# Kernel optimization log

Measured on AMD Instinct MI355X. Metric: run time of the kernel, lower is better.

## Reference

```python
import jax, jax.numpy as jnp
import numpy as np

VOCAB, D, A, NEG = 32000, 200, 20, 2
NUM_USERS, NUM_ITEMS = 100000, 50000
R, L, B, NNZ = 4096, 128, 1024, 20480
EPS = 1e-12

def _norm(x, axis):
    n = jnp.sqrt(jnp.sum(x * x, axis=axis, keepdims=True))
    return x / jnp.maximum(n, EPS)

def setup_inputs() -> dict:
    key = jax.random.key(0)
    ks = jax.random.split(key, 20)
    rows_u = jax.random.randint(ks[5], (NNZ,), 0, B)
    cols_u = jax.random.randint(ks[6], (NNZ,), 0, R)
    rows_i = jax.random.randint(ks[7], (NNZ,), 0, B)
    cols_i = jax.random.randint(ks[8], (NNZ,), 0, R)
    return {
        "historical_review": jax.random.randint(ks[0], (R, L), 0, VOCAB),
        "neg_review": jax.random.randint(ks[1], (R * NEG, L), 0, VOCAB),
        "user": jax.random.randint(ks[2], (B,), 0, NUM_USERS),
        "item": jax.random.randint(ks[3], (B,), 0, NUM_ITEMS),
        "label": jax.random.uniform(ks[4], (B,), jnp.float32, 1.0, 5.0),
        "user_histor_index": jnp.stack([rows_u, cols_u]),
        "user_histor_value": jax.random.uniform(ks[9], (NNZ,), jnp.float32),
        "item_histor_index": jnp.stack([rows_i, cols_i]),
        "item_histor_value": jax.random.uniform(ks[10], (NNZ,), jnp.float32),
        "word_emb": jax.random.normal(ks[11], (VOCAB, D), jnp.float32),
        "Wm": jax.random.normal(ks[12], (D, D), jnp.float32) * 0.05,
        "Ww": jax.random.normal(ks[13], (A, D), jnp.float32) * 0.05,
        "bw": jnp.zeros((A,), jnp.float32),
        "Wt": jax.random.normal(ks[14], (D, A), jnp.float32) * 0.05,
        "fc_w": jax.random.uniform(ks[15], (1, 2 * D), jnp.float32, -0.05, 0.05),
        "fc_b": jnp.zeros((1,), jnp.float32),
        "fm_V": jax.random.uniform(ks[16], (2 * D, 10), jnp.float32, -0.05, 0.05),
        "b_users": jax.random.uniform(ks[17], (NUM_USERS, 1), jnp.float32, 0.0, 0.1),
        "b_items": jax.random.uniform(ks[18], (NUM_ITEMS, 1), jnp.float32, 0.0, 0.1),
    }

def reference(historical_review, neg_review, user, item, label,
              user_histor_index, user_histor_value,
              item_histor_index, item_histor_value,
              word_emb, Wm, Ww, bw, Wt, fc_w, fc_b, fm_V, b_users, b_items):
    # ABAE attention over each review
    e_w = word_emb[historical_review]              # (R, L, D)
    y_s = jnp.mean(e_w, axis=1)                    # (R, D)
    z_n = jnp.mean(word_emb[neg_review], axis=1)   # (R*NEG, D)
    dx = jnp.einsum('rld,rd->rl', e_w @ Wm.T, y_s) # (R, L)
    ax = jax.nn.softmax(dx, axis=1)
    # Faithful to source: view(R, D, L) is a raw reshape, not a transpose.
    z_s = jnp.einsum('rdl,rl->rd', e_w.reshape(R, D, L), ax)  # (R, D)
    p_t = z_s @ Ww.T + bw                          # (R, A)
    r_s = p_t @ Wt.T                               # (R, D)
    # cosine margin ranking loss
    c1 = jnp.sum(_norm(r_s, 1) * _norm(z_s, 1), axis=-1)      # (R,)
    c1 = jnp.repeat(c1, NEG)                                   # (R*NEG,)
    c2 = jnp.sum(_norm(z_n.reshape(R, NEG, D), 2) * _norm(r_s, 1)[:, None, :], axis=-1).reshape(-1)
    abae_out_loss = jax.nn.relu(c2 - c1 + 1.0)     # margin=1, target=+1
    J_loss = jnp.mean(abae_out_loss)
    # aspect-matrix orthogonality regularizer
    Tn = _norm(Wt, 0)                              # normalize columns (dim=0)
    U_loss = jnp.mean((Tn.T @ Tn - jnp.eye(A, dtype=Wt.dtype)) ** 2)
    # sparse (B, R) @ (R, D) aggregation via segment_sum
    user_aspect_embed = jax.ops.segment_sum(
        user_histor_value[:, None] * r_s[user_histor_index[1]],
        user_histor_index[0], num_segments=B)      # (B, D)
    item_aspect_embed = jax.ops.segment_sum(
        item_histor_value[:, None] * r_s[item_histor_index[1]],
        item_histor_index[0], num_segments=B)      # (B, D)
    input_vec = jnp.concatenate([user_aspect_embed, item_aspect_embed], axis=1)  # (B, 2D)
    fm_linear = input_vec @ fc_w.T + fc_b          # (B, 1)
    fm_i1 = (input_vec @ fm_V) ** 2
    fm_i2 = (input_vec ** 2) @ (fm_V ** 2)
    # NOTE: faithful to source, the quadratic term is summed over the whole batch (scalar)
    fm_output = 0.5 * jnp.sum(fm_i1 - fm_i2) + fm_linear + b_users[user] + b_items[item]
    prediction = fm_output.squeeze(1)              # (B,)
    rating_loss = (prediction - label) ** 2
    mse_loss = jnp.mean(rating_loss)
    obj_loss = mse_loss + 0.01 * J_loss + 0.01 * U_loss
    return (obj_loss, rating_loss, abae_out_loss, prediction, user_aspect_embed, item_aspect_embed)
```

## Files before the change

### kernel.cpp

```cpp
#include <hip/hip_runtime.h>
#include <hip/hip_fp16.h>
#include <math.h>

#define R_TOT 4096
#define L_LEN 128
#define D_DIM 200
#define A_DIM 20
#define NEGK  2
#define B_SZ  1024
#define NNZ_C 20480
#define RN_TOT (R_TOT*NEGK)
#define S_TOT (R_TOT + RN_TOT)
#define VOCAB_C 32000
#define VHALF 16000
#define EPS_ 1e-12f
#define SLOT_CAP 64
#define NBUCK_BLK 160

__device__ __forceinline__ float4 unpack4(const uint2 u) {
  union { unsigned v; __half2 h; } c0, c1;
  c0.v = u.x; c1.v = u.y;
  const float2 f0 = __half22float2(c0.h);
  const float2 f1 = __half22float2(c1.h);
  return make_float4(f0.x, f0.y, f1.x, f1.y);
}

typedef _Float16 h2v __attribute__((ext_vector_type(2)));
__device__ __forceinline__ float fdot2u(unsigned a, unsigned b, float c) {
  union { unsigned u; h2v h; } ua, ub;
  ua.u = a; ub.u = b;
  return __builtin_amdgcn_fdot2(ua.h, ub.h, c, false);
}
__device__ __forceinline__ float dot8f(const uint4 q, const uint4 w, float c) {
  float s = c;
  s = fdot2u(q.x, w.x, s); s = fdot2u(q.y, w.y, s);
  s = fdot2u(q.z, w.z, s); s = fdot2u(q.w, w.w, s);
  return s;
}

#define DPPI(old_, src_, ctrl, rmask) \
  __builtin_amdgcn_update_dpp(old_, src_, ctrl, rmask, 0xf, false)

__device__ __forceinline__ float dpp_sum32(float s) {
  s += __int_as_float(DPPI(0, __float_as_int(s), 0x111, 0xf));
  s += __int_as_float(DPPI(0, __float_as_int(s), 0x112, 0xf));
  s += __int_as_float(DPPI(0, __float_as_int(s), 0x114, 0xf));
  s += __int_as_float(DPPI(0, __float_as_int(s), 0x118, 0xf));
  s += __int_as_float(DPPI(0, __float_as_int(s), 0x142, 0xa));
  return s;
}
__device__ __forceinline__ float dpp_sum64(float s) {
  s = dpp_sum32(s);
  s += __int_as_float(DPPI(0, __float_as_int(s), 0x143, 0xc));
  return s;
}
__device__ __forceinline__ float dpp_max64(float s) {
  s = fmaxf(s, __int_as_float(DPPI(__float_as_int(s), __float_as_int(s), 0x111, 0xf)));
  s = fmaxf(s, __int_as_float(DPPI(__float_as_int(s), __float_as_int(s), 0x112, 0xf)));
  s = fmaxf(s, __int_as_float(DPPI(__float_as_int(s), __float_as_int(s), 0x114, 0xf)));
  s = fmaxf(s, __int_as_float(DPPI(__float_as_int(s), __float_as_int(s), 0x118, 0xf)));
  s = fmaxf(s, __int_as_float(DPPI(__float_as_int(s), __float_as_int(s), 0x142, 0xa)));
  s = fmaxf(s, __int_as_float(DPPI(__float_as_int(s), __float_as_int(s), 0x143, 0xc)));
  return s;
}

__global__ __launch_bounds__(256) void k_cast(
    const float* __restrict__ emb, ushort* __restrict__ emb_h, int* __restrict__ cnt)
{
  if (blockIdx.x == 0) {
    for (int i = threadIdx.x; i < 2*B_SZ; i += 256) cnt[i] = 0;
  }
  const int idx = blockIdx.x*256 + threadIdx.x;
  if (idx < (VOCAB_C*D_DIM)/4) {
    const float4 v = reinterpret_cast<const float4*>(emb)[idx];
    ushort4 o;
    o.x = __half_as_ushort(__float2half(v.x));
    o.y = __half_as_ushort(__float2half(v.y));
    o.z = __half_as_ushort(__float2half(v.z));
    o.w = __half_as_ushort(__float2half(v.w));
    reinterpret_cast<ushort4*>(emb_h)[idx] = o;
  }
}

#define ACC8M(Q, M) { \
  const float4 e0_ = unpack4(make_uint2((Q).x,(Q).y)); \
  const float4 e1_ = unpack4(make_uint2((Q).z,(Q).w)); \
  sA.x = fmaf(M, e0_.x, sA.x); sA.y = fmaf(M, e0_.y, sA.y); \
  sA.z = fmaf(M, e0_.z, sA.z); sA.w = fmaf(M, e0_.w, sA.w); \
  sB.x = fmaf(M, e1_.x, sB.x); sB.y = fmaf(M, e1_.y, sB.y); \
  sB.z = fmaf(M, e1_.z, sB.z); sB.w = fmaf(M, e1_.w, sB.w); }

__global__ __launch_bounds__(256, 8) void k_means_phase(
    const int* __restrict__ hist, const int* __restrict__ neg,
    const ushort* __restrict__ emb_h,
    float* __restrict__ ys_all, float* __restrict__ zn_all,
    const int* __restrict__ uidx, const float* __restrict__ uval,
    const int* __restrict__ iidx, const float* __restrict__ ival,
    int* __restrict__ cnt, int* __restrict__ scol, float* __restrict__ sval,
    int lo, int finalize)
{
  const int sb = blockIdx.x;
  const int tid = threadIdx.x;

  if (sb >= S_TOT) {
    const int g = (sb - S_TOT)*256 + tid;
    if (g < NNZ_C) {
      const int b = uidx[g];
      const int slot = atomicAdd(&cnt[b], 1);
      if (slot < SLOT_CAP) {
        scol[b*SLOT_CAP + slot] = uidx[NNZ_C + g];
        sval[b*SLOT_CAP + slot] = uval[g];
      }
    } else {
      const int g2 = g - NNZ_C;
      const int b = iidx[g2];
      const int slot = atomicAdd(&cnt[B_SZ + b], 1);
      if (slot < SLOT_CAP) {
        scol[(B_SZ + b)*SLOT_CAP + slot] = iidx[NNZ_C + g2];
        sval[(B_SZ + b)*SLOT_CAP + slot] = ival[g2];
      }
    }
    return;
  }

  __shared__ int widx[L_LEN];
  __shared__ __align__(16) float part[8][D_DIM];
  const bool is_pos = (sb < R_TOT);
  const int* src = is_pos ? (hist + (size_t)sb*L_LEN)
                          : (neg + (size_t)(sb - R_TOT)*L_LEN);
  if (tid < L_LEN) widx[tid] = src[tid];
  __syncthreads();

  const int c5 = tid & 31;
  const int j  = tid >> 5;
  float4 sA = {0.f,0.f,0.f,0.f}, sB = {0.f,0.f,0.f,0.f};
  if (c5 < 25) {
    const size_t coff = 8*c5;
    #pragma unroll
    for (int half = 0; half < 2; ++half) {
      const int base = j + 64*half;
      int   wv_[8]; float m_[8];
      #pragma unroll
      for (int k = 0; k < 8; ++k) {
        const int w = widx[base + 8*k];
        const bool in = ((unsigned)(w - lo) < (unsigned)VHALF);
        wv_[k] = in ? w : 0;
        m_[k]  = in ? 1.f : 0.f;
      }
      const uint4 q0 = *reinterpret_cast<const uint4*>(emb_h + (size_t)wv_[0]*D_DIM + coff);
      const uint4 q1 = *reinterpret_cast<const uint4*>(emb_h + (size_t)wv_[1]*D_DIM + coff);
      const uint4 q2 = *reinterpret_cast<const uint4*>(emb_h + (size_t)wv_[2]*D_DIM + coff);
      const uint4 q3 = *reinterpret_cast<const uint4*>(emb_h + (size_t)wv_[3]*D_DIM + coff);
      const uint4 q4 = *reinterpret_cast<const uint4*>(emb_h + (size_t)wv_[4]*D_DIM + coff);
      const uint4 q5 = *reinterpret_cast<const uint4*>(emb_h + (size_t)wv_[5]*D_DIM + coff);
      const uint4 q6 = *reinterpret_cast<const uint4*>(emb_h + (size_t)wv_[6]*D_DIM + coff);
      const uint4 q7 = *reinterpret_cast<const uint4*>(emb_h + (size_t)wv_[7]*D_DIM + coff);
      ACC8M(q0, m_[0]) ACC8M(q1, m_[1]) ACC8M(q2, m_[2]) ACC8M(q3, m_[3])
      ACC8M(q4, m_[4]) ACC8M(q5, m_[5]) ACC8M(q6, m_[6]) ACC8M(q7, m_[7])
    }
    *reinterpret_cast<float4*>(&part[j][8*c5])     = sA;
    *reinterpret_cast<float4*>(&part[j][8*c5 + 4]) = sB;
  }
  __syncthreads();
  float* dst = is_pos ? (ys_all + (size_t)sb*D_DIM)
                      : (zn_all + (size_t)(sb - R_TOT)*D_DIM);
  if (tid < D_DIM) {
    float a = 0.f;
    #pragma unroll
    for (int j2 = 0; j2 < 8; ++j2) a += part[j2][tid];
    if (finalize) dst[tid] = (dst[tid] + a) * (1.0f/128.0f);
    else          dst[tid] = a;
  }
}

#define KB_RT 16
__global__ __launch_bounds__(256, 2) void k_matvec(
    const float* __restrict__ ys_all, const float* __restrict__ Wm,
    ushort* __restrict__ vvh)
{
  __shared__ float ysl[KB_RT][D_DIM];
  const int r0 = blockIdx.x * KB_RT;
  const int tid = threadIdx.x;
  for (int i = tid; i < KB_RT*D_DIM; i += 256)
    ysl[i / D_DIM][i % D_DIM] = ys_all[(size_t)r0*D_DIM + i];
  __syncthreads();
  if (tid < D_DIM) {
    float acc[KB_RT];
    #pragma unroll
    for (int r = 0; r < KB_RT; ++r) acc[r] = 0.f;
    #pragma unroll 4
    for (int k = 0; k < D_DIM; ++k) {
      const float w = Wm[k*D_DIM + tid];
      #pragma unroll
      for (int r = 0; r < KB_RT; ++r) acc[r] += ysl[r][k] * w;
    }
    #pragma unroll
    for (int r = 0; r < KB_RT; ++r)
      vvh[(size_t)(r0 + r)*D_DIM + tid] = __half_as_ushort(__float2half(acc[r]));
  }
}

__global__ __launch_bounds__(512, 8) void k_attn(
    const int* __restrict__ hist, const ushort* __restrict__ emb_h,
    const ushort* __restrict__ vvh,
    const float* __restrict__ Ww, const float* __restrict__ bw,
    const float* __restrict__ Wt, const float* __restrict__ zn_all,
    float* __restrict__ rs_out, float* __restrict__ abae)
{
  __shared__ __align__(16) float part[D_DIM][17];
  __shared__ __align__(16) float ax[L_LEN];
  __shared__ __align__(16) ushort axh[L_LEN];
  __shared__ __align__(16) float zs[D_DIM];
  __shared__ __align__(16) float ubuf[240];
  int*   widx  = reinterpret_cast<int*>(ubuf);
  float* ptile = ubuf;
  float* red   = ubuf + 160;

  const int r = blockIdx.x;
  const int tid = threadIdx.x, lane = tid & 63, wv = tid >> 6;
  const int c5 = tid & 31;
  const int j  = tid >> 5;
  const bool act = (c5 < 25);
  const int coff = 8*c5;

  if (tid < L_LEN) widx[tid] = hist[r*L_LEN + tid];
  uint4 v8u = make_uint4(0,0,0,0);
  if (act) v8u = *reinterpret_cast<const uint4*>(vvh + (size_t)r*D_DIM + coff);
  __syncthreads();

  uint4 q0,q1,q2,q3,q4,q5,q6,q7;
  q0=q1=q2=q3=q4=q5=q6=q7=make_uint4(0,0,0,0);
  float zn0 = 0.f, zn1 = 0.f;
  float p0=0.f,p1=0.f,p2=0.f,p3=0.f,p4=0.f,p5=0.f,p6=0.f,p7=0.f;
  if (act) {
    q0 = *reinterpret_cast<const uint4*>(emb_h + (size_t)widx[j +   0]*D_DIM + coff);
    q1 = *reinterpret_cast<const uint4*>(emb_h + (size_t)widx[j +  16]*D_DIM + coff);
    q2 = *reinterpret_cast<const uint4*>(emb_h + (size_t)widx[j +  32]*D_DIM + coff);
    q3 = *reinterpret_cast<const uint4*>(emb_h + (size_t)widx[j +  48]*D_DIM + coff);
    q4 = *reinterpret_cast<const uint4*>(emb_h + (size_t)widx[j +  64]*D_DIM + coff);
    q5 = *reinterpret_cast<const uint4*>(emb_h + (size_t)widx[j +  80]*D_DIM + coff);
    q6 = *reinterpret_cast<const uint4*>(emb_h + (size_t)widx[j +  96]*D_DIM + coff);
    q7 = *reinterpret_cast<const uint4*>(emb_h + (size_t)widx[j + 112]*D_DIM + coff);
  }
  if (tid < D_DIM) {
    zn0 = zn_all[(size_t)(2*r)*D_DIM + tid];
    zn1 = zn_all[(size_t)(2*r + 1)*D_DIM + tid];
  }
  if (act) {
    p0 = dot8f(q0, v8u, 0.f); p1 = dot8f(q1, v8u, 0.f);
    p2 = dot8f(q2, v8u, 0.f); p3 = dot8f(q3, v8u, 0.f);
    p4 = dot8f(q4, v8u, 0.f); p5 = dot8f(q5, v8u, 0.f);
    p6 = dot8f(q6, v8u, 0.f); p7 = dot8f(q7, v8u, 0.f);
  }
  p0 = dpp_sum32(p0); p1 = dpp_sum32(p1); p2 = dpp_sum32(p2); p3 = dpp_sum32(p3);
  p4 = dpp_sum32(p4); p5 = dpp_sum32(p5); p6 = dpp_sum32(p6); p7 = dpp_sum32(p7);
  if (c5 == 31) {
    ax[j]      = p0; ax[j + 16]  = p1; ax[j + 32]  = p2; ax[j + 48]  = p3;
    ax[j + 64] = p4; ax[j + 80]  = p5; ax[j + 96]  = p6; ax[j + 112] = p7;
  }
  __syncthreads();

  float mx = fmaxf(ax[lane], ax[lane + 64]);
  mx = dpp_max64(mx);
  const float M = __int_as_float(__builtin_amdgcn_readlane(__float_as_int(mx), 63));

  if (tid < L_LEN) {
    const float e = expf(ax[tid] - M);
    axh[tid] = __half_as_ushort(__float2half(e));
    const float s = dpp_sum64(e);
    if (lane == 63) red[1 + wv] = s;
  }
  __syncthreads();

  if (act) {
    const int Y  = 25*j + c5;
    const int l0 = (8*Y) & 127;
    const int v0 = Y >> 4;
    const int sl = Y & 15;
    const uint4 ax8u = *reinterpret_cast<const uint4*>(axh + l0);
    part[v0 +   0][sl] = dot8f(q0, ax8u, 0.f);
    part[v0 +  25][sl] = dot8f(q1, ax8u, 0.f);
    part[v0 +  50][sl] = dot8f(q2, ax8u, 0.f);
    part[v0 +  75][sl] = dot8f(q3, ax8u, 0.f);
    part[v0 + 100][sl] = dot8f(q4, ax8u, 0.f);
    part[v0 + 125][sl] = dot8f(q5, ax8u, 0.f);
    part[v0 + 150][sl] = dot8f(q6, ax8u, 0.f);
    part[v0 + 175][sl] = dot8f(q7, ax8u, 0.f);
  }
  __syncthreads();

  if (tid < D_DIM) {
    const float Sinv = 1.0f / (red[1] + red[2]);
    float s = 0.f;
    #pragma unroll
    for (int i = 0; i < 16; ++i) s += part[tid][i];
    zs[tid] = s * Sinv;
  }
  __syncthreads();

  if (tid < 160) {
    const int a = tid % 20, jj = tid / 20;
    float s = 0.f;
    #pragma unroll
    for (int ii = 0; ii < 25; ++ii) {
      const int d = jj + 8*ii;
      s += zs[d] * Ww[a*D_DIM + d];
    }
    ptile[tid] = s;
  }
  __syncthreads();
  if (tid < A_DIM) {
    float s = bw[tid];
    #pragma unroll
    for (int jj = 0; jj < 8; ++jj) s += ptile[jj*20 + tid];
    red[2 + tid] = s;
  }
  __syncthreads();

  float rsd = 0.f, zsd = 0.f;
  if (tid < D_DIM) {
    float acc = 0.f;
    #pragma unroll
    for (int a = 0; a < A_DIM; ++a) acc += red[2+a] * Wt[tid*A_DIM + a];
    rsd = acc; zsd = zs[tid];
    rs_out[(size_t)r*D_DIM + tid] = acc;
  } else { zn0 = 0.f; zn1 = 0.f; }
  float a0 = dpp_sum64(rsd*rsd), a1 = dpp_sum64(zsd*zsd), a2 = dpp_sum64(rsd*zsd);
  float b0 = dpp_sum64(zn0*zn0), b1 = dpp_sum64(zn0*rsd);
  float b2 = dpp_sum64(zn1*zn1), b3 = dpp_sum64(zn1*rsd);
  if (lane == 63) {
    red[22 + 0*8 + wv] = a0; red[22 + 1*8 + wv] = a1; red[22 + 2*8 + wv] = a2;
    red[22 + 3*8 + wv] = b0; red[22 + 4*8 + wv] = b1;
    red[22 + 5*8 + wv] = b2; red[22 + 6*8 + wv] = b3;
  }
  __syncthreads();

  if (tid < 64) {
    const int qi = tid >> 3, k = tid & 7;
    float v = (qi < 7) ? red[22 + 8*qi + k] : 0.f;
    v += __shfl_xor(v, 1); v += __shfl_xor(v, 2); v += __shfl_xor(v, 4);
    const float s0 = __shfl(v, 0),  s1 = __shfl(v, 8),  s2 = __shfl(v, 16);
    const float t0 = __shfl(v, 24), t1 = __shfl(v, 32);
    const float t2 = __shfl(v, 40), t3 = __shfl(v, 48);
    if (tid == 0) {
      const float nr = fmaxf(sqrtf(s0), EPS_);
      const float nz = fmaxf(sqrtf(s1), EPS_);
      const float c1 = s2 / (nr * nz);
      const float c2a = t1 / (fmaxf(sqrtf(t0), EPS_) * nr);
      const float c2b = t3 / (fmaxf(sqrtf(t2), EPS_) * nr);
      abae[2*r]     = fmaxf(c2a - c1 + 1.0f, 0.0f);
      abae[2*r + 1] = fmaxf(c2b - c1 + 1.0f, 0.0f);
    }
  }
}

__global__ __launch_bounds__(512) void k_aggfm(
    const int* __restrict__ cnt, const int* __restrict__ scol,
    const float* __restrict__ sval, const float* __restrict__ rs,
    const float* __restrict__ fcw, const float* __restrict__ V,
    const float* __restrict__ Wt, const float* __restrict__ abae,
    float* __restrict__ uae, float* __restrict__ iae,
    float* __restrict__ linb, float* __restrict__ quadb,
    float* __restrict__ uj)
{
  __shared__ __align__(16) float ivec[2*D_DIM];
  __shared__ float redw[8];
  __shared__ float qpart[10];
  __shared__ float cninvS[A_DIM];
  const int b = blockIdx.x;
  const int tid = threadIdx.x, lane = tid & 63, wv = tid >> 6;

  if (b == B_SZ) {
    if (tid < 400) {
      const int a = tid / 20, c = tid % 20;
      float dot = 0.f;
      #pragma unroll 4
      for (int d = 0; d < D_DIM; ++d) dot += Wt[d*A_DIM + a] * Wt[d*A_DIM + c];
      ivec[tid] = dot;
    }
    __syncthreads();
    if (tid < A_DIM) cninvS[tid] = 1.0f / fmaxf(sqrtf(ivec[tid*21]), EPS_);
    __syncthreads();
    float u = 0.f;
    if (tid < 400) {
      const int a = tid / 20, c = tid % 20;
      const float g = ivec[tid]*cninvS[a]*cninvS[c] - (a==c ? 1.0f : 0.0f);
      u = g*g;
    }
    #pragma unroll
    for (int o = 32; o > 0; o >>= 1) u += __shfl_xor(u, o);
    if (lane == 0) redw[wv] = u;
    __syncthreads();
    if (tid == 0) {
      float s = 0.f;
      #pragma unroll
      for (int i = 0; i < 8; ++i) s += redw[i];
      uj[0] = s;
    }
    return;
  }
  if (b == B_SZ + 1) {
    float s = 0.f;
    for (int i = tid; i < RN_TOT; i += 512) s += abae[i];
    #pragma unroll
    for (int o = 32; o > 0; o >>= 1) s += __shfl_xor(s, o);
    if (lane == 0) redw[wv] = s;
    __syncthreads();
    if (tid == 0) {
      float t = 0.f;
      #pragma unroll
      for (int i = 0; i < 8; ++i) t += redw[i];
      uj[1] = t;
    }
    return;
  }

  if (tid < D_DIM) {
    int n = cnt[b]; n = n < SLOT_CAP ? n : SLOT_CAP;
    const int* cols = scol + (size_t)b*SLOT_CAP;
    const float* vals = sval + (size_t)b*SLOT_CAP;
    float acc = 0.f;
    for (int j = 0; j < n; ++j) acc += vals[j] * rs[(size_t)cols[j]*D_DIM + tid];
    ivec[tid] = acc;
    uae[(size_t)b*D_DIM + tid] = acc;
  } else if (tid >= 256 && tid < 256 + D_DIM) {
    const int t = tid - 256;
    int n = cnt[B_SZ + b]; n = n < SLOT_CAP ? n : SLOT_CAP;
    const int* cols = scol + (size_t)(B_SZ + b)*SLOT_CAP;
    const float* vals = sval + (size_t)(B_SZ + b)*SLOT_CAP;
    float acc = 0.f;
    for (int j = 0; j < n; ++j) acc += vals[j] * rs[(size_t)cols[j]*D_DIM + t];
    ivec[D_DIM + t] = acc;
    iae[(size_t)b*D_DIM + t] = acc;
  }
  __syncthreads();

  float lv = 0.f;
  if (tid < 2*D_DIM) lv = ivec[tid] * fcw[tid];
  #pragma unroll
  for (int o = 32; o > 0; o >>= 1) lv += __shfl_xor(lv, o);
  if (lane == 0) redw[wv] = lv;

  {
    const int k = wv;
    float s1 = 0.f, s2 = 0.f;
    for (int f = lane; f < 2*D_DIM; f += 64) {
      const float x = ivec[f];
      const float vk = V[f*10 + k];
      s1 += x*vk; s2 += x*x*vk*vk;
    }
    #pragma unroll
    for (int o = 32; o > 0; o >>= 1) { s1 += __shfl_xor(s1,o); s2 += __shfl_xor(s2,o); }
    if (lane == 0) qpart[k] = s1*s1 - s2;
  }
  if (wv < 2) {
    const int k = 8 + wv;
    float s1 = 0.f, s2 = 0.f;
    for (int f = lane; f < 2*D_DIM; f += 64) {
      const float x = ivec[f];
      const float vk = V[f*10 + k];
      s1 += x*vk; s2 += x*x*vk*vk;
    }
    #pragma unroll
    for (int o = 32; o > 0; o >>= 1) { s1 += __shfl_xor(s1,o); s2 += __shfl_xor(s2,o); }
    if (lane == 0) qpart[k] = s1*s1 - s2;
  }
  __syncthreads();
  if (tid == 0) {
    float lin = 0.f;
    #pragma unroll
    for (int i = 0; i < 8; ++i) lin += redw[i];
    float q = 0.f;
    #pragma unroll
    for (int i = 0; i < 10; ++i) q += qpart[i];
    linb[b] = lin; quadb[b] = q;
  }
}

__global__ __launch_bounds__(1024) void k_final2(
    const float* __restrict__ quadb, const float* __restrict__ linb,
    const float* __restrict__ fcb, const int* __restrict__ user,
    const int* __restrict__ item, const float* __restrict__ busers,
    const float* __restrict__ bitems, const float* __restrict__ label,
    const float* __restrict__ uj,
    float* __restrict__ pred, float* __restrict__ rl, float* __restrict__ obj)
{
  __shared__ float sA[16], sC[16];
  __shared__ float quad_s;
  const int tid = threadIdx.x;
  const int lane = tid & 63;
  const int wv = tid >> 6;

  float q = quadb[tid];
  #pragma unroll
  for (int o = 32; o > 0; o >>= 1) q += __shfl_xor(q, o);
  if (lane == 0) sA[wv] = q;
  __syncthreads();
  if (wv == 0) {
    float s = (lane < 16) ? sA[lane] : 0.f;
    #pragma unroll
    for (int o = 32; o > 0; o >>= 1) s += __shfl_xor(s, o);
    if (lane == 0) quad_s = s;
  }
  __syncthreads();

  const float p = 0.5f*quad_s + linb[tid] + fcb[0]
                + busers[user[tid]] + bitems[item[tid]];
  pred[tid] = p;
  const float dd = p - label[tid];
  const float myrl = dd*dd;
  rl[tid] = myrl;

  float ms = myrl;
  #pragma unroll
  for (int o = 32; o > 0; o >>= 1) ms += __shfl_xor(ms, o);
  if (lane == 0) sC[wv] = ms;
  __syncthreads();
  if (tid == 0) {
    float Ms = 0.f;
    for (int i = 0; i < 16; ++i) Ms += sC[i];
    obj[0] = Ms/1024.0f + 0.01f*(uj[1]/8192.0f) + 0.01f*(uj[0]/400.0f);
  }
}

extern "C" void kernel_launch(void* const* d_in, const int* in_sizes, int n_in,
                              void* d_out, int out_size, void* d_ws, size_t ws_size,
                              hipStream_t stream) {
  const int*   hist   = (const int*)  d_in[0];
  const int*   neg    = (const int*)  d_in[1];
  const int*   user   = (const int*)  d_in[2];
  const int*   item   = (const int*)  d_in[3];
  const float* label  = (const float*)d_in[4];
  const int*   uidx   = (const int*)  d_in[5];
  const float* uval   = (const float*)d_in[6];
  const int*   iidx   = (const int*)  d_in[7];
  const float* ival   = (const float*)d_in[8];
  const float* emb    = (const float*)d_in[9];
  const float* Wm     = (const float*)d_in[10];
  const float* Ww     = (const float*)d_in[11];
  const float* bw     = (const float*)d_in[12];
  const float* Wt     = (const float*)d_in[13];
  const float* fcw    = (const float*)d_in[14];
  const float* fcb    = (const float*)d_in[15];
  const float* V      = (const float*)d_in[16];
  const float* busers = (const float*)d_in[17];
  const float* bitems = (const float*)d_in[18];

  float* out  = (float*)d_out;
  float* obj  = out;
  float* rl   = out + 1;
  float* abae = out + 1 + B_SZ;
  float* pred = out + 1 + B_SZ + RN_TOT;
  float* uae  = pred + B_SZ;
  float* iae  = uae + (size_t)B_SZ*D_DIM;

  float* ws     = (float*)d_ws;
  float* rs     = ws;
  float* ys_all = rs + (size_t)R_TOT*D_DIM;
  float* zn_all = ys_all + (size_t)R_TOT*D_DIM;
  float* vv_reg = zn_all + (size_t)RN_TOT*D_DIM;
  float* linb   = vv_reg + (size_t)R_TOT*D_DIM;
  float* quadb  = linb + B_SZ;
  float* sval   = quadb + B_SZ;
  int*   scol   = (int*)(sval + (size_t)2*B_SZ*SLOT_CAP);
  int*   cnt    = scol + (size_t)2*B_SZ*SLOT_CAP;
  ushort* emb_h = (ushort*)(cnt + 2*B_SZ);
  ushort* vvh   = (ushort*)vv_reg;
  float*  uj    = vv_reg + (size_t)R_TOT*D_DIM/2 + 16;

  const int cast_blocks = (VOCAB_C*D_DIM/4 + 255)/256;

  k_cast       <<<cast_blocks, 256, 0, stream>>>(emb, emb_h, cnt);
  k_means_phase<<<S_TOT + NBUCK_BLK, 256, 0, stream>>>(hist, neg, emb_h,
                                                       ys_all, zn_all,
                                                       uidx, uval, iidx, ival,
                                                       cnt, scol, sval, 0, 0);
  k_means_phase<<<S_TOT, 256, 0, stream>>>(hist, neg, emb_h,
                                           ys_all, zn_all,
                                           uidx, uval, iidx, ival,
                                           cnt, scol, sval, VHALF, 1);
  k_matvec     <<<R_TOT/KB_RT, 256, 0, stream>>>(ys_all, Wm, vvh);
  k_attn       <<<R_TOT, 512, 0, stream>>>(hist, emb_h, vvh, Ww, bw, Wt,
                                           zn_all, rs, abae);
  k_aggfm      <<<B_SZ + 2, 512, 0, stream>>>(cnt, scol, sval, rs, fcw, V, Wt, abae,
                                              uae, iae, linb, quadb, uj);
  k_final2     <<<1, 1024, 0, stream>>>(quadb, linb, fcb, user, item, busers, bitems,
                                        label, uj, pred, rl, obj);
}
```

Baseline: 275.4 us.

## Fuse Wm matvec into means finalize and final reduction into aggfm via ticket

The separate k_matvec kernel is removed: each positive-review block in the finalize pass of k_means_phase now computes its own y_s·Wm row and writes the half-precision result. The k_final2 kernel is folded into k_aggfm using an atomic ticket counter, so the last block to finish computes predictions, rating losses and the objective. Together these remove two kernel launches and the global round trip of ys. In exchange, each means block reads all of Wm with no cross-row reuse, and the finalize pass now has a serial tail on the last aggfm block.

Result: slower. 295.4 us (+7.3%).

```diff
diff --git a/kernel.cpp b/kernel.cpp
--- a/kernel.cpp
+++ b/kernel.cpp
@@ -68,7 +68,7 @@
     const float* __restrict__ emb, ushort* __restrict__ emb_h, int* __restrict__ cnt)
 {
   if (blockIdx.x == 0) {
-    for (int i = threadIdx.x; i < 2*B_SZ; i += 256) cnt[i] = 0;
+    for (int i = threadIdx.x; i < 2*B_SZ + 16; i += 256) cnt[i] = 0;
   }
   const int idx = blockIdx.x*256 + threadIdx.x;
   if (idx < (VOCAB_C*D_DIM)/4) {
@@ -92,8 +92,9 @@
 
 __global__ __launch_bounds__(256, 8) void k_means_phase(
     const int* __restrict__ hist, const int* __restrict__ neg,
-    const ushort* __restrict__ emb_h,
+    const ushort* __restrict__ emb_h, const float* __restrict__ Wm,
     float* __restrict__ ys_all, float* __restrict__ zn_all,
+    ushort* __restrict__ vvh,
     const int* __restrict__ uidx, const float* __restrict__ uval,
     const int* __restrict__ iidx, const float* __restrict__ ival,
     int* __restrict__ cnt, int* __restrict__ scol, float* __restrict__ sval,
@@ -125,6 +126,7 @@
 
   __shared__ int widx[L_LEN];
   __shared__ __align__(16) float part[8][D_DIM];
+  __shared__ __align__(16) float ysm[D_DIM];
   const bool is_pos = (sb < R_TOT);
   const int* src = is_pos ? (hist + (size_t)sb*L_LEN)
                           : (neg + (size_t)(sb - R_TOT)*L_LEN);
@@ -162,41 +164,41 @@
     *reinterpret_cast<float4*>(&part[j][8*c5 + 4]) = sB;
   }
   __syncthreads();
-  float* dst = is_pos ? (ys_all + (size_t)sb*D_DIM)
-                      : (zn_all + (size_t)(sb - R_TOT)*D_DIM);
-  if (tid < D_DIM) {
-    float a = 0.f;
-    #pragma unroll
-    for (int j2 = 0; j2 < 8; ++j2) a += part[j2][tid];
-    if (finalize) dst[tid] = (dst[tid] + a) * (1.0f/128.0f);
-    else          dst[tid] = a;
-  }
-}
-
-#define KB_RT 16
-__global__ __launch_bounds__(256, 2) void k_matvec(
-    const float* __restrict__ ys_all, const float* __restrict__ Wm,
-    ushort* __restrict__ vvh)
-{
-  __shared__ float ysl[KB_RT][D_DIM];
-  const int r0 = blockIdx.x * KB_RT;
-  const int tid = threadIdx.x;
-  for (int i = tid; i < KB_RT*D_DIM; i += 256)
-    ysl[i / D_DIM][i % D_DIM] = ys_all[(size_t)r0*D_DIM + i];
-  __syncthreads();
-  if (tid < D_DIM) {
-    float acc[KB_RT];
-    #pragma unroll
-    for (int r = 0; r < KB_RT; ++r) acc[r] = 0.f;
-    #pragma unroll 4
-    for (int k = 0; k < D_DIM; ++k) {
-      const float w = Wm[k*D_DIM + tid];
-      #pragma unroll
-      for (int r = 0; r < KB_RT; ++r) acc[r] += ysl[r][k] * w;
-    }
-    #pragma unroll
-    for (int r = 0; r < KB_RT; ++r)
-      vvh[(size_t)(r0 + r)*D_DIM + tid] = __half_as_ushort(__float2half(acc[r]));
+
+  if (!finalize) {
+    float* dst = is_pos ? (ys_all + (size_t)sb*D_DIM)
+                        : (zn_all + (size_t)(sb - R_TOT)*D_DIM);
+    if (tid < D_DIM) {
+      float a = 0.f;
+      #pragma unroll
+      for (int j2 = 0; j2 < 8; ++j2) a += part[j2][tid];
+      dst[tid] = a;
+    }
+    return;
+  }
+
+  if (is_pos) {
+    if (tid < D_DIM) {
+      float a = 0.f;
+      #pragma unroll
+      for (int j2 = 0; j2 < 8; ++j2) a += part[j2][tid];
+      ysm[tid] = (ys_all[(size_t)sb*D_DIM + tid] + a) * (1.0f/128.0f);
+    }
+    __syncthreads();
+    if (tid < D_DIM) {
+      float acc = 0.f;
+      #pragma unroll 4
+      for (int d = 0; d < D_DIM; ++d) acc += ysm[d] * Wm[d*D_DIM + tid];
+      vvh[(size_t)sb*D_DIM + tid] = __half_as_ushort(__float2half(acc));
+    }
+  } else {
+    if (tid < D_DIM) {
+      float a = 0.f;
+      #pragma unroll
+      for (int j2 = 0; j2 < 8; ++j2) a += part[j2][tid];
+      float* dst = zn_all + (size_t)(sb - R_TOT)*D_DIM;
+      dst[tid] = (dst[tid] + a) * (1.0f/128.0f);
+    }
   }
 }
 
@@ -359,14 +361,20 @@
     const float* __restrict__ sval, const float* __restrict__ rs,
     const float* __restrict__ fcw, const float* __restrict__ V,
     const float* __restrict__ Wt, const float* __restrict__ abae,
+    const float* __restrict__ fcb, const int* __restrict__ user,
+    const int* __restrict__ item, const float* __restrict__ busers,
+    const float* __restrict__ bitems, const float* __restrict__ label,
     float* __restrict__ uae, float* __restrict__ iae,
     float* __restrict__ linb, float* __restrict__ quadb,
-    float* __restrict__ uj)
+    float* __restrict__ uj, int* __restrict__ done,
+    float* __restrict__ pred, float* __restrict__ rl, float* __restrict__ obj)
 {
   __shared__ __align__(16) float ivec[2*D_DIM];
   __shared__ float redw[8];
   __shared__ float qpart[10];
   __shared__ float cninvS[A_DIM];
+  __shared__ int ticket_s;
+  __shared__ float quad_s;
   const int b = blockIdx.x;
   const int tid = threadIdx.x, lane = tid & 63, wv = tid >> 6;
 
@@ -397,9 +405,7 @@
       for (int i = 0; i < 8; ++i) s += redw[i];
       uj[0] = s;
     }
-    return;
-  }
-  if (b == B_SZ + 1) {
+  } else if (b == B_SZ + 1) {
     float s = 0.f;
     for (int i = tid; i < RN_TOT; i += 512) s += abae[i];
     #pragma unroll
@@ -412,113 +418,107 @@
       for (int i = 0; i < 8; ++i) t += redw[i];
       uj[1] = t;
     }
-    return;
-  }
-
-  if (tid < D_DIM) {
-    int n = cnt[b]; n = n < SLOT_CAP ? n : SLOT_CAP;
-    const int* cols = scol + (size_t)b*SLOT_CAP;
-    const float* vals = sval + (size_t)b*SLOT_CAP;
-    float acc = 0.f;
-    for (int j = 0; j < n; ++j) acc += vals[j] * rs[(size_t)cols[j]*D_DIM + tid];
-    ivec[tid] = acc;
-    uae[(size_t)b*D_DIM + tid] = acc;
-  } else if (tid >= 256 && tid < 256 + D_DIM) {
-    const int t = tid - 256;
-    int n = cnt[B_SZ + b]; n = n < SLOT_CAP ? n : SLOT_CAP;
-    const int* cols = scol + (size_t)(B_SZ + b)*SLOT_CAP;
-    const float* vals = sval + (size_t)(B_SZ + b)*SLOT_CAP;
-    float acc = 0.f;
-    for (int j = 0; j < n; ++j) acc += vals[j] * rs[(size_t)cols[j]*D_DIM + t];
-    ivec[D_DIM + t] = acc;
-    iae[(size_t)b*D_DIM + t] = acc;
-  }
-  __syncthreads();
-
-  float lv = 0.f;
-  if (tid < 2*D_DIM) lv = ivec[tid] * fcw[tid];
+  } else {
+    if (tid < D_DIM) {
+      int n = cnt[b]; n = n < SLOT_CAP ? n : SLOT_CAP;
+      const int* cols = scol + (size_t)b*SLOT_CAP;
+      const float* vals = sval + (size_t)b*SLOT_CAP;
+      float acc = 0.f;
+      for (int j = 0; j < n; ++j) acc += vals[j] * rs[(size_t)cols[j]*D_DIM + tid];
+      ivec[tid] = acc;
+      uae[(size_t)b*D_DIM + tid] = acc;
+    } else if (tid >= 256 && tid < 256 + D_DIM) {
+      const int t = tid - 256;
+      int n = cnt[B_SZ + b]; n = n < SLOT_CAP ? n : SLOT_CAP;
+      const int* cols = scol + (size_t)(B_SZ + b)*SLOT_CAP;
+      const float* vals = sval + (size_t)(B_SZ + b)*SLOT_CAP;
+      float acc = 0.f;
+      for (int j = 0; j < n; ++j) acc += vals[j] * rs[(size_t)cols[j]*D_DIM + t];
+      ivec[D_DIM + t] = acc;
+      iae[(size_t)b*D_DIM + t] = acc;
+    }
+    __syncthreads();
+
+    float lv = 0.f;
+    if (tid < 2*D_DIM) lv = ivec[tid] * fcw[tid];
+    #pragma unroll
+    for (int o = 32; o > 0; o >>= 1) lv += __shfl_xor(lv, o);
+    if (lane == 0) redw[wv] = lv;
+
+    {
+      const int k = wv;
+      float s1 = 0.f, s2 = 0.f;
+      for (int f = lane; f < 2*D_DIM; f += 64) {
+        const float x = ivec[f];
+        const float vk = V[f*10 + k];
+        s1 += x*vk; s2 += x*x*vk*vk;
+      }
+      #pragma unroll
+      for (int o = 32; o > 0; o >>= 1) { s1 += __shfl_xor(s1,o); s2 += __shfl_xor(s2,o); }
+      if (lane == 0) qpart[k] = s1*s1 - s2;
+    }
+    if (wv < 2) {
+      const int k = 8 + wv;
+      float s1 = 0.f, s2 = 0.f;
+      for (int f = lane; f < 2*D_DIM; f += 64) {
+        const float x = ivec[f];
+        const float vk = V[f*10 + k];
+        s1 += x*vk; s2 += x*x*vk*vk;
+      }
+      #pragma unroll
+      for (int o = 32; o > 0; o >>= 1) { s1 += __shfl_xor(s1,o); s2 += __shfl_xor(s2,o); }
+      if (lane == 0) qpart[k] = s1*s1 - s2;
+    }
+    __syncthreads();
+    if (tid == 0) {
+      float lin = 0.f;
+      #pragma unroll
+      for (int i = 0; i < 8; ++i) lin += redw[i];
+      float q = 0.f;
+      #pragma unroll
+      for (int i = 0; i < 10; ++i) q += qpart[i];
+      linb[b] = lin; quadb[b] = q;
+    }
+  }
+
+  __syncthreads();
+  if (tid == 0) {
+    __threadfence();
+    ticket_s = atomicAdd(done, 1);
+  }
+  __syncthreads();
+  if (ticket_s != B_SZ + 1) return;
+  __threadfence();
+
+  float q = quadb[tid] + quadb[tid + 512];
+  q = dpp_sum64(q);
+  if (lane == 63) redw[wv] = q;
+  __syncthreads();
+  if (tid == 0) {
+    float s = 0.f;
+    #pragma unroll
+    for (int i = 0; i < 8; ++i) s += redw[i];
+    quad_s = s;
+  }
+  __syncthreads();
+
+  float ms = 0.f;
+  const float qs = 0.5f * quad_s, fb = fcb[0];
   #pragma unroll
-  for (int o = 32; o > 0; o >>= 1) lv += __shfl_xor(lv, o);
-  if (lane == 0) redw[wv] = lv;
-
-  {
-    const int k = wv;
-    float s1 = 0.f, s2 = 0.f;
-    for (int f = lane; f < 2*D_DIM; f += 64) {
-      const float x = ivec[f];
-      const float vk = V[f*10 + k];
-      s1 += x*vk; s2 += x*x*vk*vk;
-    }
-    #pragma unroll
-    for (int o = 32; o > 0; o >>= 1) { s1 += __shfl_xor(s1,o); s2 += __shfl_xor(s2,o); }
-    if (lane == 0) qpart[k] = s1*s1 - s2;
-  }
-  if (wv < 2) {
-    const int k = 8 + wv;
-    float s1 = 0.f, s2 = 0.f;
-    for (int f = lane; f < 2*D_DIM; f += 64) {
-      const float x = ivec[f];
-      const float vk = V[f*10 + k];
-      s1 += x*vk; s2 += x*x*vk*vk;
-    }
-    #pragma unroll
-    for (int o = 32; o > 0; o >>= 1) { s1 += __shfl_xor(s1,o); s2 += __shfl_xor(s2,o); }
-    if (lane == 0) qpart[k] = s1*s1 - s2;
-  }
-  __syncthreads();
-  if (tid == 0) {
-    float lin = 0.f;
-    #pragma unroll
-    for (int i = 0; i < 8; ++i) lin += redw[i];
-    float q = 0.f;
-    #pragma unroll
-    for (int i = 0; i < 10; ++i) q += qpart[i];
-    linb[b] = lin; quadb[b] = q;
-  }
-}
-
-__global__ __launch_bounds__(1024) void k_final2(
-    const float* __restrict__ quadb, const float* __restrict__ linb,
-    const float* __restrict__ fcb, const int* __restrict__ user,
-    const int* __restrict__ item, const float* __restrict__ busers,
-    const float* __restrict__ bitems, const float* __restrict__ label,
-    const float* __restrict__ uj,
-    float* __restrict__ pred, float* __restrict__ rl, float* __restrict__ obj)
-{
-  __shared__ float sA[16], sC[16];
-  __shared__ float quad_s;
-  const int tid = threadIdx.x;
-  const int lane = tid & 63;
-  const int wv = tid >> 6;
-
-  float q = quadb[tid];
-  #pragma unroll
-  for (int o = 32; o > 0; o >>= 1) q += __shfl_xor(q, o);
-  if (lane == 0) sA[wv] = q;
-  __syncthreads();
-  if (wv == 0) {
-    float s = (lane < 16) ? sA[lane] : 0.f;
-    #pragma unroll
-    for (int o = 32; o > 0; o >>= 1) s += __shfl_xor(s, o);
-    if (lane == 0) quad_s = s;
-  }
-  __syncthreads();
-
-  const float p = 0.5f*quad_s + linb[tid] + fcb[0]
-                + busers[user[tid]] + bitems[item[tid]];
-  pred[tid] = p;
-  const float dd = p - label[tid];
-  const float myrl = dd*dd;
-  rl[tid] = myrl;
-
-  float ms = myrl;
-  #pragma unroll
-  for (int o = 32; o > 0; o >>= 1) ms += __shfl_xor(ms, o);
-  if (lane == 0) sC[wv] = ms;
+  for (int i = tid; i < B_SZ; i += 512) {
+    const float p = qs + linb[i] + fb + busers[user[i]] + bitems[item[i]];
+    pred[i] = p;
+    const float dd = p - label[i];
+    rl[i] = dd*dd;
+    ms += dd*dd;
+  }
+  ms = dpp_sum64(ms);
+  if (lane == 63) redw[wv] = ms;
   __syncthreads();
   if (tid == 0) {
     float Ms = 0.f;
-    for (int i = 0; i < 16; ++i) Ms += sC[i];
+    #pragma unroll
+    for (int i = 0; i < 8; ++i) Ms += redw[i];
     obj[0] = Ms/1024.0f + 0.01f*(uj[1]/8192.0f) + 0.01f*(uj[0]/400.0f);
   }
 }
@@ -564,26 +564,26 @@
   float* sval   = quadb + B_SZ;
   int*   scol   = (int*)(sval + (size_t)2*B_SZ*SLOT_CAP);
   int*   cnt    = scol + (size_t)2*B_SZ*SLOT_CAP;
-  ushort* emb_h = (ushort*)(cnt + 2*B_SZ);
+  int*   done   = cnt + 2*B_SZ;
+  ushort* emb_h = (ushort*)(cnt + 2*B_SZ + 16);
   ushort* vvh   = (ushort*)vv_reg;
   float*  uj    = vv_reg + (size_t)R_TOT*D_DIM/2 + 16;
 
   const int cast_blocks = (VOCAB_C*D_DIM/4 + 255)/256;
 
   k_cast       <<<cast_blocks, 256, 0, stream>>>(emb, emb_h, cnt);
-  k_means_phase<<<S_TOT + NBUCK_BLK, 256, 0, stream>>>(hist, neg, emb_h,
-                                                       ys_all, zn_all,
+  k_means_phase<<<S_TOT + NBUCK_BLK, 256, 0, stream>>>(hist, neg, emb_h, Wm,
+                                                       ys_all, zn_all, vvh,
                                                        uidx, uval, iidx, ival,
                                                        cnt, scol, sval, 0, 0);
-  k_means_phase<<<S_TOT, 256, 0, stream>>>(hist, neg, emb_h,
-                                           ys_all, zn_all,
+  k_means_phase<<<S_TOT, 256, 0, stream>>>(hist, neg, emb_h, Wm,
+                                           ys_all, zn_all, vvh,
                                            uidx, uval, iidx, ival,
                                            cnt, scol, sval, VHALF, 1);
-  k_matvec     <<<R_TOT/KB_RT, 256, 0, stream>>>(ys_all, Wm, vvh);
   k_attn       <<<R_TOT, 512, 0, stream>>>(hist, emb_h, vvh, Ww, bw, Wt,
                                            zn_all, rs, abae);
   k_aggfm      <<<B_SZ + 2, 512, 0, stream>>>(cnt, scol, sval, rs, fcw, V, Wt, abae,
-                                              uae, iae, linb, quadb, uj);
-  k_final2     <<<1, 1024, 0, stream>>>(quadb, linb, fcb, user, item, busers, bitems,
-                                        label, uj, pred, rl, obj);
-}
+                                              fcb, user, item, busers, bitems, label,
+                                              uae, iae, linb, quadb, uj, done,
+                                              pred, rl, obj);
+}
```
